# Performance work log

Hardware: AMD Instinct MI355X
Metric: run time of the kernel (lower is better)

The kernel has to match this reference:

```python
import jax, jax.numpy as jnp
import numpy as np

F = 256          # number of features (input_size)
H1, H2, H3 = 128, 64, 32
OUT = 1          # output_size


def setup_inputs() -> dict:
    key = jax.random.key(0)
    ks = jax.random.split(key, 10)
    B = 8192
    # Kaiming-uniform-ish small init; exact init doesn't matter for a math reference.
    def w(k, shape, fan_in):
        lim = 1.0 / np.sqrt(fan_in)
        return jax.random.uniform(k, shape, jnp.float32, -lim, lim)
    return {
        "x": jax.random.normal(ks[0], (B, F), dtype=jnp.float32),
        "W1": w(ks[1], (F, H1), 1),          # Linear(1 -> H1) per feature
        "b1": w(ks[2], (F, H1), 1),
        "W2": w(ks[3], (F, H1, H2), H1),
        "b2": w(ks[4], (F, H2), H1),
        "W3": w(ks[5], (F, H2, H3), H2),
        "b3": w(ks[6], (F, H3), H2),
        "W4": w(ks[7], (F, H3, OUT), H3),
        "b4": w(ks[8], (F, OUT), H3),
        "bias": jnp.zeros((OUT,), dtype=jnp.float32),
    }


def reference(x, W1, b1, W2, b2, W3, b3, W4, b4, bias):
    # Fused form of the per-feature FeatureNN loop (eval mode: dropout = identity).
    # Layer 1: scalar input per feature -> H1
    h = jax.nn.relu(x[:, :, None] * W1[None, :, :] + b1[None, :, :])   # [B,F,H1]
    h = jax.nn.relu(jnp.einsum('bfh,fhk->bfk', h, W2) + b2[None])      # [B,F,H2]
    h = jax.nn.relu(jnp.einsum('bfh,fhk->bfk', h, W3) + b3[None])      # [B,F,H3]
    f_out = jnp.einsum('bfh,fhk->bfk', h, W4) + b4[None]               # [B,F,OUT]
    # torch.cat(dim=1).sum(dim=1, keepdim=True): sum over features and output cols
    out = jnp.sum(f_out, axis=(1, 2), keepdims=False)[:, None] + bias[None, :]
    return out  # [B, OUT] with OUT==1
```

## Files before the change

### kernel.cpp

```cpp
#include <hip/hip_runtime.h>
#include <math.h>


#define NF   256
#define NH1  128
#define NH2  64
#define NH3  32
#define NB   8192

#define NRANK 129
#define ROW4  17
#define ROWH  136

typedef float    f32x16 __attribute__((ext_vector_type(16)));
typedef unsigned u32x4  __attribute__((ext_vector_type(4)));
typedef _Float16 h16x2  __attribute__((ext_vector_type(2)));
typedef _Float16 h16x8  __attribute__((ext_vector_type(8)));

__device__ __forceinline__ unsigned pkh2(unsigned sw, unsigned sb, h16x2 xh) {
    h16x2 r = __builtin_elementwise_fma(xh, __builtin_bit_cast(h16x2, sw),
                                            __builtin_bit_cast(h16x2, sb));
    h16x2 hz = {(_Float16)0.f, (_Float16)0.f};
    return __builtin_bit_cast(unsigned, __builtin_elementwise_max(r, hz));
}

__global__ __launch_bounds__(256) void init_out_kernel(float* __restrict__ out,
                                                       const float* __restrict__ bias) {
    int i = blockIdx.x * 256 + threadIdx.x;
    if (i < NB) out[i] = bias[0];
}

__global__ __launch_bounds__(1024, 4) void nam_fused(
    const float* __restrict__ x,
    const float* __restrict__ W1, const float* __restrict__ b1,
    const float* __restrict__ W2, const float* __restrict__ b2,
    const float* __restrict__ W3, const float* __restrict__ b3,
    const float* __restrict__ W4, const float* __restrict__ b4,
    float* __restrict__ out)
{
    __shared__ u32x4 SP4[NRANK * ROW4];
    __shared__ float tkey[NH1];
    __shared__ int   tidx[NH1];
    __shared__ float w1s[NH1], b1s[NH1];
    __shared__ float Pbw[8][NH2], Pbb[8][NH2], Pdw[8][NH2], Pdb[8][NH2];

    const int f    = blockIdx.x >> 1;
    const int half = blockIdx.x & 1;
    const int t = (int)threadIdx.x;
    _Float16* SPh = (_Float16*)SP4;

    const float* __restrict__ gw2 = W2 + (size_t)f * NH1 * NH2;
    if (t < NH1) {
        float w  = W1[f * NH1 + t];
        float bb = b1[f * NH1 + t];
        w1s[t] = w; b1s[t] = bb;
        tkey[t] = (w != 0.0f) ? (-bb / w) : INFINITY;
        tidx[t] = t;
    }
    __syncthreads();

    for (int size = 2; size <= NH1; size <<= 1) {
        for (int stride = size >> 1; stride > 0; stride >>= 1) {
            if (t < 64) {
                int pos = ((t / stride) * (stride << 1)) + (t % stride);
                int par = pos + stride;
                bool up = ((pos & size) == 0);
                float a = tkey[pos], c = tkey[par];
                int  ia = tidx[pos], ic = tidx[par];
                if ((a > c) == up) {
                    tkey[pos] = c; tkey[par] = a;
                    tidx[pos] = ic; tidx[par] = ia;
                }
            }
            __syncthreads();
        }
    }

    if (t < 512) {
        const int k = t & 63, c = t >> 6;
        float bw = 0.0f, bbp = 0.0f, dw = 0.0f, db = 0.0f;
        #pragma unroll 4
        for (int i = 0; i < 16; ++i) {
            int j = c * 16 + i;
            float w = w1s[j], bv = b1s[j], w2v = gw2[j * NH2 + k];
            if (w < 0.0f) { bw = fmaf(w, w2v, bw); bbp = fmaf(bv, w2v, bbp); }
            else if (w == 0.0f && bv > 0.0f) { bbp = fmaf(bv, w2v, bbp); }
            int jj = tidx[c * 16 + i];
            float ww = w1s[jj], bv2 = b1s[jj], w2x = gw2[jj * NH2 + k];
            float s = (ww > 0.0f) ? 1.0f : ((ww < 0.0f) ? -1.0f : 0.0f);
            dw = fmaf(s * ww,  w2x, dw);
            db = fmaf(s * bv2, w2x, db);
        }
        Pbw[c][k] = bw; Pbb[c][k] = bbp; Pdw[c][k] = dw; Pdb[c][k] = db;
    }
    __syncthreads();
    if (t < 512) {
        const int k = t & 63, c = t >> 6;
        float accw = 0.0f;
        float accb = b2[f * NH2 + k];
        #pragma unroll
        for (int c2 = 0; c2 < 8; ++c2) { accw += Pbw[c2][k]; accb += Pbb[c2][k]; }
        for (int c2 = 0; c2 < c; ++c2) { accw += Pdw[c2][k]; accb += Pdb[c2][k]; }
        if (c == 0) {
            SPh[k]      = (_Float16)accw;
            SPh[64 + k] = (_Float16)accb;
        }
        #pragma unroll 4
        for (int i = 0; i < 16; ++i) {
            int r = c * 16 + i;
            int j = tidx[r];
            float w = w1s[j], bv = b1s[j], w2v = gw2[j * NH2 + k];
            float s = (w > 0.0f) ? 1.0f : ((w < 0.0f) ? -1.0f : 0.0f);
            accw = fmaf(s * w,  w2v, accw);
            accb = fmaf(s * bv, w2v, accb);
            SPh[(r + 1) * ROWH + k]      = (_Float16)accw;
            SPh[(r + 1) * ROWH + 64 + k] = (_Float16)accb;
        }
    }
    __syncthreads();

    const int lane = t & 63, wv = t >> 6;
    const int n = lane & 31, q2 = lane >> 5;

    const float* __restrict__ w3g = W3 + f * NH2 * NH3;
    h16x8 A0, A1, A2, A3;
    #pragma unroll
    for (int j = 0; j < 8; ++j) {
        int kk = q2 * 8 + j;
        A0[j] = (_Float16)w3g[kk * NH3 + n];
        A1[j] = (_Float16)w3g[(kk + 16) * NH3 + n];
        A2[j] = (_Float16)w3g[(kk + 32) * NH3 + n];
        A3[j] = (_Float16)w3g[(kk + 48) * NH3 + n];
    }
    float b3r[16], w4r[16];
    #pragma unroll
    for (int reg = 0; reg < 16; ++reg) {
        int row = (reg & 3) + 8 * (reg >> 2) + 4 * q2;
        b3r[reg] = b3[f * NH3 + row];
        w4r[reg] = W4[f * NH3 + row];
    }
    const float b4f = b4[f];
    const float t63 = tkey[63], t31 = tkey[31], t95 = tkey[95];
    const float t15 = tkey[15], t47 = tkey[47], t79 = tkey[79], t111 = tkey[111];

    #pragma unroll 1
    for (int round = 0; round < 8; ++round) {
        const int base = half * 4096 + (round * 16 + wv) * 32;
        const float xv = x[(size_t)(base + n) * NF + f];

        int r = (t63 < xv) ? 64 : 0;
        {
            float l1 = (r & 64) ? t95 : t31;
            if (l1 < xv) r += 32;
            float m0 = (r & 64) ? t79  : t15;
            float m1 = (r & 64) ? t111 : t47;
            float l2 = (r & 32) ? m1 : m0;
            if (l2 < xv) r += 16;
        }
        #pragma unroll
        for (int s = 8; s > 0; s >>= 1)
            if (tkey[r + s - 1] < xv) r += s;

        const int ro = r * ROW4;
        u32x4 SW0 = SP4[ro + q2],      SW1 = SP4[ro + 2 + q2];
        u32x4 SW2 = SP4[ro + 4 + q2],  SW3 = SP4[ro + 6 + q2];
        u32x4 SB0 = SP4[ro + 8 + q2],  SB1 = SP4[ro + 10 + q2];
        u32x4 SB2 = SP4[ro + 12 + q2], SB3 = SP4[ro + 14 + q2];

        const h16x2 xh = {(_Float16)xv, (_Float16)xv};
        u32x4 d0, d1, d2, d3;
        d0.x = pkh2(SW0.x, SB0.x, xh); d0.y = pkh2(SW0.y, SB0.y, xh);
        d0.z = pkh2(SW0.z, SB0.z, xh); d0.w = pkh2(SW0.w, SB0.w, xh);
        d1.x = pkh2(SW1.x, SB1.x, xh); d1.y = pkh2(SW1.y, SB1.y, xh);
        d1.z = pkh2(SW1.z, SB1.z, xh); d1.w = pkh2(SW1.w, SB1.w, xh);
        d2.x = pkh2(SW2.x, SB2.x, xh); d2.y = pkh2(SW2.y, SB2.y, xh);
        d2.z = pkh2(SW2.z, SB2.z, xh); d2.w = pkh2(SW2.w, SB2.w, xh);
        d3.x = pkh2(SW3.x, SB3.x, xh); d3.y = pkh2(SW3.y, SB3.y, xh);
        d3.z = pkh2(SW3.z, SB3.z, xh); d3.w = pkh2(SW3.w, SB3.w, xh);
        h16x8 B0 = __builtin_bit_cast(h16x8, d0);
        h16x8 B1 = __builtin_bit_cast(h16x8, d1);
        h16x8 B2 = __builtin_bit_cast(h16x8, d2);
        h16x8 B3 = __builtin_bit_cast(h16x8, d3);

        f32x16 acc;
        #pragma unroll
        for (int reg = 0; reg < 16; ++reg) acc[reg] = b3r[reg];
        acc = __builtin_amdgcn_mfma_f32_32x32x16_f16(A0, B0, acc, 0, 0, 0);
        acc = __builtin_amdgcn_mfma_f32_32x32x16_f16(A1, B1, acc, 0, 0, 0);
        acc = __builtin_amdgcn_mfma_f32_32x32x16_f16(A2, B2, acc, 0, 0, 0);
        acc = __builtin_amdgcn_mfma_f32_32x32x16_f16(A3, B3, acc, 0, 0, 0);

        float p = 0.0f;
        #pragma unroll
        for (int reg = 0; reg < 16; ++reg)
            p = fmaf(fmaxf(acc[reg], 0.0f), w4r[reg], p);
        p += __shfl_xor(p, 32);
        if (lane < 32) atomicAdd(&out[base + lane], p + b4f);
    }
}

extern "C" void kernel_launch(void* const* d_in, const int* in_sizes, int n_in,
                              void* d_out, int out_size, void* d_ws, size_t ws_size,
                              hipStream_t stream) {
    const float* x    = (const float*)d_in[0];
    const float* W1   = (const float*)d_in[1];
    const float* b1   = (const float*)d_in[2];
    const float* W2   = (const float*)d_in[3];
    const float* b2   = (const float*)d_in[4];
    const float* W3   = (const float*)d_in[5];
    const float* b3   = (const float*)d_in[6];
    const float* W4   = (const float*)d_in[7];
    const float* b4   = (const float*)d_in[8];
    const float* bias = (const float*)d_in[9];
    float* out = (float*)d_out;

    init_out_kernel<<<NB / 256, 256, 0, stream>>>(out, bias);
    nam_fused<<<NF * 2, 1024, 0, stream>>>(x, W1, b1, W2, b2,
                                           W3, b3, W4, b4, out);
}
```

Before: 129.8 us.

## Split table build into separate kernel and spread batch over more blocks

Per-feature table construction (the sort and prefix tables) now runs once per feature in a dedicated kernel that writes to workspace, and the output init is folded into it. The main kernel loads the precomputed tables from global memory and splits the batch into four quarters with 512-thread blocks. Before, each of the two half-batch blocks per feature rebuilt the same table. This removes that duplicated work and raises block-level parallelism, at the cost of a global round-trip for the tables and a dependency between the two kernels.

```diff
diff --git a/kernel.cpp b/kernel.cpp
--- a/kernel.cpp
+++ b/kernel.cpp
@@ -11,6 +11,7 @@
 #define NRANK 129
 #define ROW4  17
 #define ROWH  136
+#define TBLDW 8960
 
 typedef float    f32x16 __attribute__((ext_vector_type(16)));
 typedef unsigned u32x4  __attribute__((ext_vector_type(4)));
@@ -24,19 +25,11 @@
     return __builtin_bit_cast(unsigned, __builtin_elementwise_max(r, hz));
 }
 
-__global__ __launch_bounds__(256) void init_out_kernel(float* __restrict__ out,
-                                                       const float* __restrict__ bias) {
-    int i = blockIdx.x * 256 + threadIdx.x;
-    if (i < NB) out[i] = bias[0];
-}
-
-__global__ __launch_bounds__(1024, 4) void nam_fused(
-    const float* __restrict__ x,
+__global__ __launch_bounds__(512) void build_tables(
     const float* __restrict__ W1, const float* __restrict__ b1,
     const float* __restrict__ W2, const float* __restrict__ b2,
-    const float* __restrict__ W3, const float* __restrict__ b3,
-    const float* __restrict__ W4, const float* __restrict__ b4,
-    float* __restrict__ out)
+    const float* __restrict__ bias, float* __restrict__ out,
+    unsigned* __restrict__ ws)
 {
     __shared__ u32x4 SP4[NRANK * ROW4];
     __shared__ float tkey[NH1];
@@ -44,10 +37,12 @@
     __shared__ float w1s[NH1], b1s[NH1];
     __shared__ float Pbw[8][NH2], Pbb[8][NH2], Pdw[8][NH2], Pdb[8][NH2];
 
-    const int f    = blockIdx.x >> 1;
-    const int half = blockIdx.x & 1;
+    const int f = blockIdx.x;
     const int t = (int)threadIdx.x;
     _Float16* SPh = (_Float16*)SP4;
+
+    const int gid = f * 512 + t;
+    if (gid < NB) out[gid] = bias[0];
 
     const float* __restrict__ gw2 = W2 + (size_t)f * NH1 * NH2;
     if (t < NH1) {
@@ -76,7 +71,7 @@
         }
     }
 
-    if (t < 512) {
+    {
         const int k = t & 63, c = t >> 6;
         float bw = 0.0f, bbp = 0.0f, dw = 0.0f, db = 0.0f;
         #pragma unroll 4
@@ -94,7 +89,7 @@
         Pbw[c][k] = bw; Pbb[c][k] = bbp; Pdw[c][k] = dw; Pdb[c][k] = db;
     }
     __syncthreads();
-    if (t < 512) {
+    {
         const int k = t & 63, c = t >> 6;
         float accw = 0.0f;
         float accb = b2[f * NH2 + k];
@@ -119,6 +114,37 @@
     }
     __syncthreads();
 
+    unsigned* __restrict__ wsf = ws + (size_t)f * TBLDW;
+    if (t < NH1) wsf[t] = __float_as_uint(tkey[t]);
+    const u32x4* src = (const u32x4*)SP4;
+    u32x4* dst = (u32x4*)(wsf + NH1);
+    #pragma unroll 2
+    for (int i = t; i < NRANK * ROW4; i += 512) dst[i] = src[i];
+}
+
+__global__ __launch_bounds__(512, 8) void nam_main(
+    const float* __restrict__ x,
+    const float* __restrict__ W3, const float* __restrict__ b3,
+    const float* __restrict__ W4, const float* __restrict__ b4,
+    const unsigned* __restrict__ ws,
+    float* __restrict__ out)
+{
+    __shared__ u32x4 SP4[NRANK * ROW4];
+    __shared__ float tkey[NH1];
+
+    const int f  = blockIdx.x >> 2;
+    const int qt = blockIdx.x & 3;
+    const int t  = (int)threadIdx.x;
+
+    const unsigned* __restrict__ wsf = ws + (size_t)f * TBLDW;
+    if (t < NH1) tkey[t] = __uint_as_float(wsf[t]);
+    {
+        const u32x4* src = (const u32x4*)(wsf + NH1);
+        #pragma unroll 2
+        for (int i = t; i < NRANK * ROW4; i += 512) SP4[i] = src[i];
+    }
+    __syncthreads();
+
     const int lane = t & 63, wv = t >> 6;
     const int n = lane & 31, q2 = lane >> 5;
 
@@ -145,7 +171,7 @@
 
     #pragma unroll 1
     for (int round = 0; round < 8; ++round) {
-        const int base = half * 4096 + (round * 16 + wv) * 32;
+        const int base = qt * 2048 + (round * 8 + wv) * 32;
         const float xv = x[(size_t)(base + n) * NF + f];
 
         int r = (t63 < xv) ? 64 : 0;
@@ -212,9 +238,9 @@
     const float* W4   = (const float*)d_in[7];
     const float* b4   = (const float*)d_in[8];
     const float* bias = (const float*)d_in[9];
-    float* out = (float*)d_out;
-
-    init_out_kernel<<<NB / 256, 256, 0, stream>>>(out, bias);
-    nam_fused<<<NF * 2, 1024, 0, stream>>>(x, W1, b1, W2, b2,
-                                           W3, b3, W4, b4, out);
-}
+    float* out   = (float*)d_out;
+    unsigned* ws = (unsigned*)d_ws;
+
+    build_tables<<<NF, 512, 0, stream>>>(W1, b1, W2, b2, bias, out, ws);
+    nam_main<<<NF * 4, 512, 0, stream>>>(x, W3, b3, W4, b4, ws, out);
+}
```

Result: slower. 232.7 us (+79.3%).
